# Performance work log

Hardware: AMD Instinct MI355X
Metric: run time of the kernel (lower is better)

The kernel has to match this reference:

```python
import jax, jax.numpy as jnp
import numpy as np

DIM = 768
HEADS = 12
HEAD_DIM = DIM // HEADS  # 64
B, T = 4, 2048


def setup_inputs() -> dict:
    key = jax.random.key(0)
    k1, k2, k3 = jax.random.split(key, 3)
    x = jax.random.normal(k1, (B, T, DIM), dtype=jnp.float32)
    w_qkv = jax.random.normal(k2, (DIM, 3 * DIM), dtype=jnp.float32) * (DIM ** -0.5)
    w_out = jax.random.normal(k3, (DIM, DIM), dtype=jnp.float32) * (DIM ** -0.5)
    b_out = jnp.zeros((DIM,), dtype=jnp.float32)
    return {"x": x, "w_qkv": w_qkv, "w_out": w_out, "b_out": b_out}


def reference(x, w_qkv, w_out, b_out):
    b, t, _ = x.shape
    # fused QKV projection (no bias)
    xp = x @ w_qkv                               # (b, t, 3*dim)
    # faithful to einops 'b t (d k h) -> k b h t d' with k=3, h=HEADS
    xp = xp.reshape(b, t, HEAD_DIM, 3, HEADS)
    qkv = jnp.transpose(xp, (3, 0, 4, 1, 2))     # (3, b, h, t, d)
    q, k, v = qkv[0], qkv[1], qkv[2]
    scores = jnp.einsum('bhid,bhjd->bhij', q, k) * (HEAD_DIM ** -0.5)
    attn = jax.nn.softmax(scores, axis=-1)
    out = jnp.einsum('bhij,bhjd->bhid', attn, v)  # (b, h, t, d)
    out = jnp.transpose(out, (0, 2, 1, 3)).reshape(b, t, HEADS * HEAD_DIM)
    return out @ w_out + b_out
```

## Files before the change

### kernel.cpp

```cpp
#include <hip/hip_runtime.h>
#include <hip/hip_bf16.h>


typedef short short8 __attribute__((ext_vector_type(8)));
typedef _Float16 half8 __attribute__((ext_vector_type(8)));
typedef _Float16 half2v __attribute__((ext_vector_type(2)));
typedef float f32x16 __attribute__((ext_vector_type(16)));
typedef unsigned int uint4v __attribute__((ext_vector_type(4)));
typedef unsigned short ushort8v __attribute__((ext_vector_type(8)));
typedef unsigned short ushort4v __attribute__((ext_vector_type(4)));
typedef unsigned short ushort;

__device__ __forceinline__ ushort f2h(float x) {
    _Float16 h = (_Float16)x;
    return __builtin_bit_cast(ushort, h);
}
__device__ __forceinline__ unsigned pk2h(float lo, float hi) {
    return __builtin_bit_cast(unsigned, __builtin_amdgcn_cvt_pkrtz(lo, hi));
}
__device__ __forceinline__ float dot2acc(unsigned pair, float acc) {
    const half2v ones = {(_Float16)1.0f, (_Float16)1.0f};
    return __builtin_amdgcn_fdot2(__builtin_bit_cast(half2v, pair), ones, acc, false);
}
__device__ __forceinline__ short8 ldfrag(const ushort* buf, int row, int slotLogical) {
    int phys = slotLogical ^ (row & 7);
    return *reinterpret_cast<const short8*>(&buf[row * 64 + phys * 8]);
}
__device__ __forceinline__ f32x16 mfma16(half8 a, half8 b, f32x16 c) {
    return __builtin_amdgcn_mfma_f32_32x32x16_f16(a, b, c, 0, 0, 0);
}
__device__ __forceinline__ half8 ldfragh(const ushort* buf, int row, int slotLogical) {
    return __builtin_bit_cast(half8, ldfrag(buf, row, slotLogical));
}
__device__ __forceinline__ void gload16(const ushort* g, ushort* l) {
    __builtin_amdgcn_global_load_lds((__attribute__((address_space(1))) void*)g,
                                     (__attribute__((address_space(3))) void*)l, 16, 0, 0);
}

__global__ __launch_bounds__(256) void prep_all(const float* __restrict__ x,
                                                const float* __restrict__ wqkv,
                                                const float* __restrict__ wout,
                                                ushort* __restrict__ Xh,
                                                ushort* __restrict__ Wt,
                                                ushort* __restrict__ Wo) {
    int b = blockIdx.x;
    if (b < 3072) {
        long i8 = (long)(b * 256 + threadIdx.x) * 8;
        float4 v0 = *reinterpret_cast<const float4*>(&x[i8]);
        float4 v1 = *reinterpret_cast<const float4*>(&x[i8 + 4]);
        float v[8] = {v0.x, v0.y, v0.z, v0.w, v1.x, v1.y, v1.z, v1.w};
        ushort8v hh;
#pragma unroll
        for (int j = 0; j < 8; ++j) hh[j] = f2h(v[j]);
        *reinterpret_cast<ushort8v*>(&Xh[i8]) = hh;
    } else if (b < 3072 + 864) {
        int id = (b - 3072) * 256 + threadIdx.x;
        int n = id % 2304;
        int oct = id / 2304;
        int g = n >> 6, d = n & 63;
        int col = d * 36 + g;
        ushort8v hh;
#pragma unroll
        for (int i = 0; i < 8; ++i) hh[i] = f2h(wqkv[(long)(8 * oct + i) * 2304 + col]);
        *reinterpret_cast<ushort8v*>(&Wt[(long)n * 768 + 8 * oct]) = hh;
    } else {
        int id = (b - 3936) * 256 + threadIdx.x;
        int n = id % 768;
        int oct = id / 768;
        ushort8v hh;
#pragma unroll
        for (int i = 0; i < 8; ++i) hh[i] = f2h(wout[(long)(8 * oct + i) * 768 + n]);
        *reinterpret_cast<ushort8v*>(&Wo[(long)n * 768 + 8 * oct]) = hh;
    }
}

__device__ __forceinline__ void gemm_core(const ushort* __restrict__ A,
                                          const ushort* __restrict__ Bt,
                                          long aBase, long bBase,
                                          ushort* sA, ushort* sB, f32x16 (&acc)[2][2]) {
    const int tid = threadIdx.x;
    const int lane = tid & 63, w = tid >> 6;
    const int c31 = lane & 31, g1 = lane >> 5;
    const int wr = w >> 1, wc = w & 1;
    const int srow_in_chunk = lane >> 3;
    for (int k0 = 0; k0 < 768; k0 += 64) {
        __syncthreads();
#pragma unroll
        for (int t = 0; t < 4; ++t) {
            int row = w * 32 + t * 8 + srow_in_chunk;
            int sl = (lane & 7) ^ (row & 7);
            long goff = (long)row * 768 + k0 + sl * 8;
            int ldst = (w * 32 + t * 8) * 64;
            gload16(&A[aBase + goff], &sA[ldst]);
            gload16(&Bt[bBase + goff], &sB[ldst]);
        }
        __syncthreads();
#pragma unroll
        for (int ks = 0; ks < 4; ++ks) {
            half8 ah[2], bh[2];
#pragma unroll
            for (int i = 0; i < 2; ++i) {
                ah[i] = ldfragh(sA, wr * 64 + i * 32 + c31, 2 * ks + g1);
                bh[i] = ldfragh(sB, wc * 64 + i * 32 + c31, 2 * ks + g1);
            }
#pragma unroll
            for (int mi = 0; mi < 2; ++mi)
#pragma unroll
                for (int nj = 0; nj < 2; ++nj)
                    acc[mi][nj] = mfma16(ah[mi], bh[nj], acc[mi][nj]);
        }
    }
}

__global__ __launch_bounds__(256) void gemm_qkv(const ushort* __restrict__ Xh,
                                                const ushort* __restrict__ Wt,
                                                ushort* __restrict__ Qf,
                                                ushort* __restrict__ Kf,
                                                ushort* __restrict__ Vt) {
    __shared__ ushort sA[128 * 64];
    __shared__ ushort sB[128 * 64];
    const int by0 = blockIdx.y * 128, bx0 = blockIdx.x * 128;
    f32x16 acc[2][2] = {};
    gemm_core(Xh, Wt, (long)by0 * 768, (long)bx0 * 768, sA, sB, acc);

    const int tid = threadIdx.x, lane = tid & 63, w = tid >> 6;
    const int c31 = lane & 31, g1 = lane >> 5;
    const int wr = w >> 1, wc = w & 1;
    const int bb = by0 >> 11, tb = by0 & 2047;
#pragma unroll
    for (int nj = 0; nj < 2; ++nj) {
        int n = bx0 + wc * 64 + nj * 32 + c31;
        int gg = n >> 6;
        int d = n & 63;
        if (gg < 24) {
            int kq = gg >= 12;
            int hh = gg - kq * 12;
            ushort* Dst = kq ? Kf : Qf;
            float sc = kq ? 0.1803368801111204f : 1.0f;
            long cb = ((long)(bb * 12 + hh) * 2048) * 64 + d;
#pragma unroll
            for (int mi = 0; mi < 2; ++mi)
#pragma unroll
                for (int r = 0; r < 16; ++r) {
                    int t = tb + wr * 64 + mi * 32 + (r & 3) + 8 * (r >> 2) + 4 * g1;
                    Dst[cb + (long)t * 64] = f2h(acc[mi][nj][r] * sc);
                }
        } else {
            int hh = gg - 24;
            long vb = ((long)(bb * 12 + hh) * 64 + d) * 2048;
#pragma unroll
            for (int mi = 0; mi < 2; ++mi)
#pragma unroll
                for (int rq = 0; rq < 4; ++rq) {
                    int tq = tb + wr * 64 + mi * 32 + 8 * rq + 4 * g1;
                    ushort4v vv;
#pragma unroll
                    for (int j = 0; j < 4; ++j) vv[j] = f2h(acc[mi][nj][4 * rq + j]);
                    *reinterpret_cast<ushort4v*>(&Vt[vb + tq]) = vv;
                }
        }
    }
}

__global__ __launch_bounds__(256) void flash_attn(const ushort* __restrict__ Qf,
                                                  const ushort* __restrict__ Kf,
                                                  const ushort* __restrict__ Vt,
                                                  ushort* __restrict__ Of) {
    __shared__ ushort Ks[3][64 * 64];
    __shared__ ushort Vs[3][64 * 64];
    const int tid = threadIdx.x;
    const int w = tid >> 6;
    const int lane = tid & 63;
    const int c = lane & 31, g1 = lane >> 5;
    const int wgid = blockIdx.x;
    const int xblk = (wgid >> 3) & 15;
    const int bh = (wgid & 7) + 8 * (wgid >> 7);
    const int t0 = xblk * 128 + w * 32;
    const long hb = (long)bh * 2048 * 64;

    half8 qh[4];
    {
        const long qrow = hb + (long)(t0 + c) * 64;
#pragma unroll
        for (int ks = 0; ks < 4; ++ks)
            qh[ks] = __builtin_bit_cast(half8, *reinterpret_cast<const short8*>(&Qf[qrow + ks * 16 + g1 * 8]));
    }

    const int r0 = tid >> 3, sl = tid & 7, r1 = r0 + 32;
    const int off0 = r0 * 64 + ((sl ^ (r0 & 7)) * 8);
    const int off1 = r1 * 64 + ((sl ^ (r1 & 7)) * 8);

    {
        short8 k00 = *reinterpret_cast<const short8*>(&Kf[hb + (long)r0 * 64 + sl * 8]);
        short8 k01 = *reinterpret_cast<const short8*>(&Kf[hb + (long)r1 * 64 + sl * 8]);
        short8 v00 = *reinterpret_cast<const short8*>(&Vt[hb + (long)r0 * 2048 + sl * 8]);
        short8 v01 = *reinterpret_cast<const short8*>(&Vt[hb + (long)r1 * 2048 + sl * 8]);
        short8 k10 = *reinterpret_cast<const short8*>(&Kf[hb + (long)(64 + r0) * 64 + sl * 8]);
        short8 k11 = *reinterpret_cast<const short8*>(&Kf[hb + (long)(64 + r1) * 64 + sl * 8]);
        short8 v10 = *reinterpret_cast<const short8*>(&Vt[hb + (long)r0 * 2048 + 64 + sl * 8]);
        short8 v11 = *reinterpret_cast<const short8*>(&Vt[hb + (long)r1 * 2048 + 64 + sl * 8]);
        *reinterpret_cast<short8*>(&Ks[0][off0]) = k00;
        *reinterpret_cast<short8*>(&Ks[0][off1]) = k01;
        *reinterpret_cast<short8*>(&Vs[0][off0]) = v00;
        *reinterpret_cast<short8*>(&Vs[0][off1]) = v01;
        *reinterpret_cast<short8*>(&Ks[1][off0]) = k10;
        *reinterpret_cast<short8*>(&Ks[1][off1]) = k11;
        *reinterpret_cast<short8*>(&Vs[1][off0]) = v10;
        *reinterpret_cast<short8*>(&Vs[1][off1]) = v11;
    }
    __syncthreads();

    const ushort* kst0 = &Kf[hb + (long)(128 + r0) * 64 + sl * 8];
    const ushort* kst1 = &Kf[hb + (long)(128 + r1) * 64 + sl * 8];
    const ushort* vst0 = &Vt[hb + (long)r0 * 2048 + 128 + sl * 8];
    const ushort* vst1 = &Vt[hb + (long)r1 * 2048 + 128 + sl * 8];

    f32x16 s0 = {}, s1 = {};
#pragma unroll
    for (int ks = 0; ks < 4; ++ks) {
        int slot = 2 * ks + g1;
        half8 k0f = ldfragh(&Ks[0][0], c, slot);
        half8 k1f = ldfragh(&Ks[0][0], 32 + c, slot);
        s0 = mfma16(k0f, qh[ks], s0);
        s1 = mfma16(k1f, qh[ks], s1);
    }

    f32x16 o0 = {}, o1 = {};
    float lrun = 0.f;
    int p = 0;

    for (int j = 0; j < 32; ++j) {
        const bool hasN1 = j + 1 < 32;
        const bool hasN2 = j + 2 < 32;
        const int p1 = (p + 1 == 3) ? 0 : p + 1;
        const int p2 = (p + 2 >= 3) ? p + 2 - 3 : p + 2;

        f32x16 n0 = {}, n1 = {};
        if (hasN1) {
            __builtin_amdgcn_s_setprio(1);
#pragma unroll
            for (int ks = 0; ks < 4; ++ks) {
                int slot = 2 * ks + g1;
                half8 k0f = ldfragh(&Ks[p1][0], c, slot);
                half8 k1f = ldfragh(&Ks[p1][0], 32 + c, slot);
                n0 = mfma16(k0f, qh[ks], n0);
                n1 = mfma16(k1f, qh[ks], n1);
            }
            __builtin_amdgcn_s_setprio(0);
        }

        short8 pk0, pk1, pv0, pv1;
        if (hasN2) {
            pk0 = *reinterpret_cast<const short8*>(kst0);
            pk1 = *reinterpret_cast<const short8*>(kst1);
            pv0 = *reinterpret_cast<const short8*>(vst0);
            pv1 = *reinterpret_cast<const short8*>(vst1);
            kst0 += 4096; kst1 += 4096;
            vst0 += 64;   vst1 += 64;
        }

#pragma unroll
        for (int r = 0; r < 16; ++r) {
            s0[r] = exp2f(s0[r]);
            s1[r] = exp2f(s1[r]);
        }

        __builtin_amdgcn_s_setprio(1);
#pragma unroll
        for (int ks = 0; ks < 4; ++ks) {
            const int b8 = (ks & 1) * 8;
            uint4v dv;
#pragma unroll
            for (int mi = 0; mi < 2; ++mi) {
                float aLo = (ks < 2) ? s0[2 * mi + b8] : s1[2 * mi + b8];
                float aHi = (ks < 2) ? s0[2 * mi + b8 + 1] : s1[2 * mi + b8 + 1];
                float bLo = (ks < 2) ? s0[2 * mi + b8 + 4] : s1[2 * mi + b8 + 4];
                float bHi = (ks < 2) ? s0[2 * mi + b8 + 5] : s1[2 * mi + b8 + 5];
                unsigned xA = pk2h(aLo, aHi);
                unsigned xB = pk2h(bLo, bHi);
                lrun = dot2acc(xA, lrun);
                lrun = dot2acc(xB, lrun);
                auto rr = __builtin_amdgcn_permlane32_swap(xA, xB, false, false);
                dv[mi] = rr[0];
                dv[2 + mi] = rr[1];
            }
            half8 pb = __builtin_bit_cast(half8, dv);
            int slot = 2 * ks + g1;
            half8 va0 = ldfragh(&Vs[p][0], c, slot);
            half8 va1 = ldfragh(&Vs[p][0], 32 + c, slot);
            o0 = mfma16(va0, pb, o0);
            o1 = mfma16(va1, pb, o1);
        }
        __builtin_amdgcn_s_setprio(0);

        if (hasN2) {
            *reinterpret_cast<short8*>(&Ks[p2][off0]) = pk0;
            *reinterpret_cast<short8*>(&Ks[p2][off1]) = pk1;
            *reinterpret_cast<short8*>(&Vs[p2][off0]) = pv0;
            *reinterpret_cast<short8*>(&Vs[p2][off1]) = pv1;
        }
        __syncthreads();

        s0 = n0; s1 = n1;
        p = p1;
    }

    const float ltot = lrun + __shfl_xor(lrun, 32);
    const float inv = 1.0f / ltot;
    const int bb = bh / 12, h = bh - bb * 12;
    const long obase = ((long)(bb * 2048 + t0 + c)) * 768 + h * 64;
#pragma unroll
    for (int m = 0; m < 4; ++m) {
        int d0 = 8 * m + 4 * g1;
        ushort4v a, b;
#pragma unroll
        for (int j = 0; j < 4; ++j) {
            a[j] = f2h(o0[4 * m + j] * inv);
            b[j] = f2h(o1[4 * m + j] * inv);
        }
        *reinterpret_cast<ushort4v*>(&Of[obase + d0]) = a;
        *reinterpret_cast<ushort4v*>(&Of[obase + 32 + d0]) = b;
    }
}

__global__ __launch_bounds__(256) void gemm_out(const ushort* __restrict__ Of,
                                                const ushort* __restrict__ Wo,
                                                const float* __restrict__ bias,
                                                float* __restrict__ Cout) {
    __shared__ ushort sA[128 * 64];
    __shared__ ushort sB[128 * 64];
    const int by0 = blockIdx.y * 128, bx0 = blockIdx.x * 128;
    f32x16 acc[2][2] = {};
    gemm_core(Of, Wo, (long)by0 * 768, (long)bx0 * 768, sA, sB, acc);

    const int tid = threadIdx.x, lane = tid & 63, w = tid >> 6;
    const int c31 = lane & 31, g1 = lane >> 5;
    const int wr = w >> 1, wc = w & 1;
#pragma unroll
    for (int nj = 0; nj < 2; ++nj) {
        int n = bx0 + wc * 64 + nj * 32 + c31;
        float bv = bias[n];
#pragma unroll
        for (int mi = 0; mi < 2; ++mi)
#pragma unroll
            for (int r = 0; r < 16; ++r) {
                int row = by0 + wr * 64 + mi * 32 + (r & 3) + 8 * (r >> 2) + 4 * g1;
                Cout[(long)row * 768 + n] = acc[mi][nj][r] + bv;
            }
    }
}

extern "C" void kernel_launch(void* const* d_in, const int* in_sizes, int n_in,
                              void* d_out, int out_size, void* d_ws, size_t ws_size,
                              hipStream_t stream) {
    const float* x     = (const float*)d_in[0];
    const float* w_qkv = (const float*)d_in[1];
    const float* w_out = (const float*)d_in[2];
    const float* b_out = (const float*)d_in[3];
    float* out = (float*)d_out;

    const long U = 12582912;
    char* p = (char*)d_ws;
    ushort* Xh = (ushort*)(p);
    ushort* Wt = (ushort*)(p + U);
    ushort* Wo = (ushort*)(p + U + 3538944);
    ushort* Qf = (ushort*)(p + U + 4718592);
    ushort* Kf = Qf + 6291456;
    ushort* Vt = Kf + 6291456;
    ushort* Of = Xh;

    prep_all  <<<4224, 256, 0, stream>>>(x, w_qkv, w_out, Xh, Wt, Wo);
    gemm_qkv  <<<dim3(18, 64), 256, 0, stream>>>(Xh, Wt, Qf, Kf, Vt);
    flash_attn<<<768, 256, 0, stream>>>(Qf, Kf, Vt, Of);
    gemm_out  <<<dim3(6, 64), 256, 0, stream>>>(Of, Wo, b_out, out);
}
```

Before: 183.2 us.

## Split attention over two key halves and combine partial outputs

Result: slower. 209.2 us (+14.1%).

```diff
diff --git a/kernel.cpp b/kernel.cpp
--- a/kernel.cpp
+++ b/kernel.cpp
@@ -15,6 +15,9 @@
     _Float16 h = (_Float16)x;
     return __builtin_bit_cast(ushort, h);
 }
+__device__ __forceinline__ float h2f(ushort u) {
+    return (float)__builtin_bit_cast(_Float16, u);
+}
 __device__ __forceinline__ unsigned pk2h(float lo, float hi) {
     return __builtin_bit_cast(unsigned, __builtin_amdgcn_cvt_pkrtz(lo, hi));
 }
@@ -31,6 +34,9 @@
 }
 __device__ __forceinline__ half8 ldfragh(const ushort* buf, int row, int slotLogical) {
     return __builtin_bit_cast(half8, ldfrag(buf, row, slotLogical));
+}
+__device__ __forceinline__ half8 ldh(const ushort* p) {
+    return __builtin_bit_cast(half8, *reinterpret_cast<const short8*>(p));
 }
 __device__ __forceinline__ void gload16(const ushort* g, ushort* l) {
     __builtin_amdgcn_global_load_lds((__attribute__((address_space(1))) void*)g,
@@ -165,25 +171,30 @@
 __global__ __launch_bounds__(256) void flash_attn(const ushort* __restrict__ Qf,
                                                   const ushort* __restrict__ Kf,
                                                   const ushort* __restrict__ Vt,
-                                                  ushort* __restrict__ Of) {
-    __shared__ ushort Ks[3][64 * 64];
-    __shared__ ushort Vs[3][64 * 64];
+                                                  ushort* __restrict__ Op0,
+                                                  ushort* __restrict__ Op1,
+                                                  float* __restrict__ lp0,
+                                                  float* __restrict__ lp1) {
+    __shared__ ushort Ks[2][64 * 64];
     const int tid = threadIdx.x;
     const int w = tid >> 6;
     const int lane = tid & 63;
     const int c = lane & 31, g1 = lane >> 5;
     const int wgid = blockIdx.x;
-    const int xblk = (wgid >> 3) & 15;
-    const int bh = (wgid & 7) + 8 * (wgid >> 7);
+    const int inner = (wgid >> 3) & 31;
+    const int xblk = inner >> 1;
+    const int kh = inner & 1;
+    const int bh = (wgid & 7) + 8 * (wgid >> 8);
     const int t0 = xblk * 128 + w * 32;
     const long hb = (long)bh * 2048 * 64;
+    const int jbase = kh * 1024;
 
     half8 qh[4];
     {
         const long qrow = hb + (long)(t0 + c) * 64;
 #pragma unroll
         for (int ks = 0; ks < 4; ++ks)
-            qh[ks] = __builtin_bit_cast(half8, *reinterpret_cast<const short8*>(&Qf[qrow + ks * 16 + g1 * 8]));
+            qh[ks] = ldh(&Qf[qrow + ks * 16 + g1 * 8]);
     }
 
     const int r0 = tid >> 3, sl = tid & 7, r1 = r0 + 32;
@@ -191,72 +202,48 @@
     const int off1 = r1 * 64 + ((sl ^ (r1 & 7)) * 8);
 
     {
-        short8 k00 = *reinterpret_cast<const short8*>(&Kf[hb + (long)r0 * 64 + sl * 8]);
-        short8 k01 = *reinterpret_cast<const short8*>(&Kf[hb + (long)r1 * 64 + sl * 8]);
-        short8 v00 = *reinterpret_cast<const short8*>(&Vt[hb + (long)r0 * 2048 + sl * 8]);
-        short8 v01 = *reinterpret_cast<const short8*>(&Vt[hb + (long)r1 * 2048 + sl * 8]);
-        short8 k10 = *reinterpret_cast<const short8*>(&Kf[hb + (long)(64 + r0) * 64 + sl * 8]);
-        short8 k11 = *reinterpret_cast<const short8*>(&Kf[hb + (long)(64 + r1) * 64 + sl * 8]);
-        short8 v10 = *reinterpret_cast<const short8*>(&Vt[hb + (long)r0 * 2048 + 64 + sl * 8]);
-        short8 v11 = *reinterpret_cast<const short8*>(&Vt[hb + (long)r1 * 2048 + 64 + sl * 8]);
-        *reinterpret_cast<short8*>(&Ks[0][off0]) = k00;
-        *reinterpret_cast<short8*>(&Ks[0][off1]) = k01;
-        *reinterpret_cast<short8*>(&Vs[0][off0]) = v00;
-        *reinterpret_cast<short8*>(&Vs[0][off1]) = v01;
-        *reinterpret_cast<short8*>(&Ks[1][off0]) = k10;
-        *reinterpret_cast<short8*>(&Ks[1][off1]) = k11;
-        *reinterpret_cast<short8*>(&Vs[1][off0]) = v10;
-        *reinterpret_cast<short8*>(&Vs[1][off1]) = v11;
-    }
+        short8 a = *reinterpret_cast<const short8*>(&Kf[hb + (long)(jbase + r0) * 64 + sl * 8]);
+        short8 b = *reinterpret_cast<const short8*>(&Kf[hb + (long)(jbase + r1) * 64 + sl * 8]);
+        *reinterpret_cast<short8*>(&Ks[0][off0]) = a;
+        *reinterpret_cast<short8*>(&Ks[0][off1]) = b;
+    }
+    const ushort* kst0 = &Kf[hb + (long)(jbase + 64 + r0) * 64 + sl * 8];
+    const ushort* kst1 = &Kf[hb + (long)(jbase + 64 + r1) * 64 + sl * 8];
+    const ushort* vp0 = &Vt[hb + (long)c * 2048 + jbase + g1 * 8];
+    const ushort* vp1 = vp0 + 32 * 2048;
     __syncthreads();
-
-    const ushort* kst0 = &Kf[hb + (long)(128 + r0) * 64 + sl * 8];
-    const ushort* kst1 = &Kf[hb + (long)(128 + r1) * 64 + sl * 8];
-    const ushort* vst0 = &Vt[hb + (long)r0 * 2048 + 128 + sl * 8];
-    const ushort* vst1 = &Vt[hb + (long)r1 * 2048 + 128 + sl * 8];
-
-    f32x16 s0 = {}, s1 = {};
-#pragma unroll
-    for (int ks = 0; ks < 4; ++ks) {
-        int slot = 2 * ks + g1;
-        half8 k0f = ldfragh(&Ks[0][0], c, slot);
-        half8 k1f = ldfragh(&Ks[0][0], 32 + c, slot);
-        s0 = mfma16(k0f, qh[ks], s0);
-        s1 = mfma16(k1f, qh[ks], s1);
-    }
 
     f32x16 o0 = {}, o1 = {};
     float lrun = 0.f;
-    int p = 0;
-
-    for (int j = 0; j < 32; ++j) {
-        const bool hasN1 = j + 1 < 32;
-        const bool hasN2 = j + 2 < 32;
-        const int p1 = (p + 1 == 3) ? 0 : p + 1;
-        const int p2 = (p + 2 >= 3) ? p + 2 - 3 : p + 2;
-
-        f32x16 n0 = {}, n1 = {};
-        if (hasN1) {
-            __builtin_amdgcn_s_setprio(1);
-#pragma unroll
-            for (int ks = 0; ks < 4; ++ks) {
-                int slot = 2 * ks + g1;
-                half8 k0f = ldfragh(&Ks[p1][0], c, slot);
-                half8 k1f = ldfragh(&Ks[p1][0], 32 + c, slot);
-                n0 = mfma16(k0f, qh[ks], n0);
-                n1 = mfma16(k1f, qh[ks], n1);
-            }
-            __builtin_amdgcn_s_setprio(0);
-        }
-
-        short8 pk0, pk1, pv0, pv1;
-        if (hasN2) {
+    int cur = 0;
+
+    for (int j = 0; j < 16; ++j) {
+        half8 vf0[4], vf1[4];
+        vf0[0] = ldh(vp0);      vf1[0] = ldh(vp1);
+        vf0[1] = ldh(vp0 + 16); vf1[1] = ldh(vp1 + 16);
+
+        f32x16 s0 = {}, s1 = {};
+        __builtin_amdgcn_s_setprio(1);
+#pragma unroll
+        for (int ks = 0; ks < 4; ++ks) {
+            int slot = 2 * ks + g1;
+            half8 k0f = ldfragh(&Ks[cur][0], c, slot);
+            half8 k1f = ldfragh(&Ks[cur][0], 32 + c, slot);
+            s0 = mfma16(k0f, qh[ks], s0);
+            s1 = mfma16(k1f, qh[ks], s1);
+        }
+        __builtin_amdgcn_s_setprio(0);
+
+        vf0[2] = ldh(vp0 + 32); vf1[2] = ldh(vp1 + 32);
+        vf0[3] = ldh(vp0 + 48); vf1[3] = ldh(vp1 + 48);
+        vp0 += 64; vp1 += 64;
+
+        short8 pk0, pk1;
+        const bool nxt = j + 1 < 16;
+        if (nxt) {
             pk0 = *reinterpret_cast<const short8*>(kst0);
             pk1 = *reinterpret_cast<const short8*>(kst1);
-            pv0 = *reinterpret_cast<const short8*>(vst0);
-            pv1 = *reinterpret_cast<const short8*>(vst1);
             kst0 += 4096; kst1 += 4096;
-            vst0 += 64;   vst1 += 64;
         }
 
 #pragma unroll
@@ -285,41 +272,67 @@
                 dv[2 + mi] = rr[1];
             }
             half8 pb = __builtin_bit_cast(half8, dv);
-            int slot = 2 * ks + g1;
-            half8 va0 = ldfragh(&Vs[p][0], c, slot);
-            half8 va1 = ldfragh(&Vs[p][0], 32 + c, slot);
-            o0 = mfma16(va0, pb, o0);
-            o1 = mfma16(va1, pb, o1);
+            o0 = mfma16(vf0[ks], pb, o0);
+            o1 = mfma16(vf1[ks], pb, o1);
         }
         __builtin_amdgcn_s_setprio(0);
 
-        if (hasN2) {
-            *reinterpret_cast<short8*>(&Ks[p2][off0]) = pk0;
-            *reinterpret_cast<short8*>(&Ks[p2][off1]) = pk1;
-            *reinterpret_cast<short8*>(&Vs[p2][off0]) = pv0;
-            *reinterpret_cast<short8*>(&Vs[p2][off1]) = pv1;
+        if (nxt) {
+            *reinterpret_cast<short8*>(&Ks[cur ^ 1][off0]) = pk0;
+            *reinterpret_cast<short8*>(&Ks[cur ^ 1][off1]) = pk1;
         }
         __syncthreads();
-
-        s0 = n0; s1 = n1;
-        p = p1;
+        cur ^= 1;
     }
 
     const float ltot = lrun + __shfl_xor(lrun, 32);
-    const float inv = 1.0f / ltot;
+    ushort* Op = kh ? Op1 : Op0;
+    float* lp = kh ? lp1 : lp0;
+    const long pbase = ((long)bh * 64) * 2048 + t0 + c;
+#pragma unroll
+    for (int r = 0; r < 16; ++r) {
+        int d0 = (r & 3) + 8 * (r >> 2) + 4 * g1;
+        Op[pbase + (long)d0 * 2048] = f2h(o0[r]);
+        Op[pbase + (long)(32 + d0) * 2048] = f2h(o1[r]);
+    }
+    if (g1 == 0) lp[(long)bh * 2048 + t0 + c] = ltot;
+}
+
+__global__ __launch_bounds__(256) void combine(const ushort* __restrict__ Op0,
+                                               const ushort* __restrict__ Op1,
+                                               const float* __restrict__ lp0,
+                                               const float* __restrict__ lp1,
+                                               ushort* __restrict__ Of) {
+    __shared__ float linv[64];
+    __shared__ ushort tile[64][72];
+    const int bh = blockIdx.x >> 5;
+    const int tb = blockIdx.x & 31;
+    const int t0 = tb * 64;
+    const int tid = threadIdx.x;
+    if (tid < 64)
+        linv[tid] = 1.0f / (lp0[(long)bh * 2048 + t0 + tid] + lp1[(long)bh * 2048 + t0 + tid]);
+    __syncthreads();
+#pragma unroll
+    for (int it = 0; it < 2; ++it) {
+        int u = tid + 256 * it;
+        int d = u & 63, tg = u >> 6;
+        long base = ((long)bh * 64 + d) * 2048 + t0 + tg * 8;
+        ushort8v a = *reinterpret_cast<const ushort8v*>(&Op0[base]);
+        ushort8v b = *reinterpret_cast<const ushort8v*>(&Op1[base]);
+#pragma unroll
+        for (int j = 0; j < 8; ++j)
+            tile[tg * 8 + j][d] = f2h((h2f(a[j]) + h2f(b[j])) * linv[tg * 8 + j]);
+    }
+    __syncthreads();
     const int bb = bh / 12, h = bh - bb * 12;
-    const long obase = ((long)(bb * 2048 + t0 + c)) * 768 + h * 64;
-#pragma unroll
-    for (int m = 0; m < 4; ++m) {
-        int d0 = 8 * m + 4 * g1;
-        ushort4v a, b;
-#pragma unroll
-        for (int j = 0; j < 4; ++j) {
-            a[j] = f2h(o0[4 * m + j] * inv);
-            b[j] = f2h(o1[4 * m + j] * inv);
-        }
-        *reinterpret_cast<ushort4v*>(&Of[obase + d0]) = a;
-        *reinterpret_cast<ushort4v*>(&Of[obase + 32 + d0]) = b;
+#pragma unroll
+    for (int it = 0; it < 2; ++it) {
+        int u = tid + 256 * it;
+        int dg = u & 7, t = u >> 3;
+        ushort8v v;
+#pragma unroll
+        for (int j = 0; j < 8; ++j) v[j] = tile[t][dg * 8 + j];
+        *reinterpret_cast<ushort8v*>(&Of[((long)(bb * 2048) + t0 + t) * 768 + h * 64 + dg * 8]) = v;
     }
 }
 
@@ -361,16 +374,21 @@
 
     const long U = 12582912;
     char* p = (char*)d_ws;
-    ushort* Xh = (ushort*)(p);
-    ushort* Wt = (ushort*)(p + U);
-    ushort* Wo = (ushort*)(p + U + 3538944);
-    ushort* Qf = (ushort*)(p + U + 4718592);
-    ushort* Kf = Qf + 6291456;
-    ushort* Vt = Kf + 6291456;
-    ushort* Of = Xh;
+    ushort* Xh  = (ushort*)(p);
+    ushort* Wt  = (ushort*)(p + U);
+    ushort* Wo  = (ushort*)(p + U + 3538944);
+    ushort* Qf  = (ushort*)(p + U + 4718592);
+    ushort* Kf  = Qf + 6291456;
+    ushort* Vt  = Kf + 6291456;
+    ushort* Op0 = Vt + 6291456;
+    ushort* Op1 = Op0 + 6291456;
+    float*  lp0 = (float*)(Op1 + 6291456);
+    float*  lp1 = lp0 + 98304;
+    ushort* Of  = Xh;
 
     prep_all  <<<4224, 256, 0, stream>>>(x, w_qkv, w_out, Xh, Wt, Wo);
     gemm_qkv  <<<dim3(18, 64), 256, 0, stream>>>(Xh, Wt, Qf, Kf, Vt);
-    flash_attn<<<768, 256, 0, stream>>>(Qf, Kf, Vt, Of);
+    flash_attn<<<1536, 256, 0, stream>>>(Qf, Kf, Vt, Op0, Op1, lp0, lp1);
+    combine   <<<1536, 256, 0, stream>>>(Op0, Op1, lp0, lp1, Of);
     gemm_out  <<<dim3(6, 64), 256, 0, stream>>>(Of, Wo, b_out, out);
 }
```

## Enlarge GEMM tiles to 256x128 with 512 threads; ping-pong flash-attn score registers

Applied to the files above, without the earlier changes.

Measured after the change: 205.5 us. 12.1% more time.

```diff
diff --git a/kernel.cpp b/kernel.cpp
--- a/kernel.cpp
+++ b/kernel.cpp
@@ -82,17 +82,20 @@
     const int lane = tid & 63, w = tid >> 6;
     const int c31 = lane & 31, g1 = lane >> 5;
     const int wr = w >> 1, wc = w & 1;
-    const int srow_in_chunk = lane >> 3;
+    const int rch = lane >> 3;
     for (int k0 = 0; k0 < 768; k0 += 64) {
         __syncthreads();
 #pragma unroll
         for (int t = 0; t < 4; ++t) {
-            int row = w * 32 + t * 8 + srow_in_chunk;
+            int row = w * 32 + t * 8 + rch;
             int sl = (lane & 7) ^ (row & 7);
-            long goff = (long)row * 768 + k0 + sl * 8;
-            int ldst = (w * 32 + t * 8) * 64;
-            gload16(&A[aBase + goff], &sA[ldst]);
-            gload16(&Bt[bBase + goff], &sB[ldst]);
+            gload16(&A[aBase + (long)row * 768 + k0 + sl * 8], &sA[(w * 32 + t * 8) * 64]);
+        }
+#pragma unroll
+        for (int t = 0; t < 2; ++t) {
+            int row = w * 16 + t * 8 + rch;
+            int sl = (lane & 7) ^ (row & 7);
+            gload16(&Bt[bBase + (long)row * 768 + k0 + sl * 8], &sB[(w * 16 + t * 8) * 64]);
         }
         __syncthreads();
 #pragma unroll
@@ -112,14 +115,14 @@
     }
 }
 
-__global__ __launch_bounds__(256) void gemm_qkv(const ushort* __restrict__ Xh,
+__global__ __launch_bounds__(512) void gemm_qkv(const ushort* __restrict__ Xh,
                                                 const ushort* __restrict__ Wt,
                                                 ushort* __restrict__ Qf,
                                                 ushort* __restrict__ Kf,
                                                 ushort* __restrict__ Vt) {
-    __shared__ ushort sA[128 * 64];
+    __shared__ ushort sA[256 * 64];
     __shared__ ushort sB[128 * 64];
-    const int by0 = blockIdx.y * 128, bx0 = blockIdx.x * 128;
+    const int by0 = blockIdx.y * 256, bx0 = blockIdx.x * 128;
     f32x16 acc[2][2] = {};
     gemm_core(Xh, Wt, (long)by0 * 768, (long)bx0 * 768, sA, sB, acc);
 
@@ -215,36 +218,46 @@
     const ushort* vst0 = &Vt[hb + (long)r0 * 2048 + 128 + sl * 8];
     const ushort* vst1 = &Vt[hb + (long)r1 * 2048 + 128 + sl * 8];
 
-    f32x16 s0 = {}, s1 = {};
-#pragma unroll
-    for (int ks = 0; ks < 4; ++ks) {
-        int slot = 2 * ks + g1;
-        half8 k0f = ldfragh(&Ks[0][0], c, slot);
-        half8 k1f = ldfragh(&Ks[0][0], 32 + c, slot);
-        s0 = mfma16(k0f, qh[ks], s0);
-        s1 = mfma16(k1f, qh[ks], s1);
+    const f32x16 kzero = {};
+
+    f32x16 s0, s1;
+    {
+        half8 k0f = ldfragh(&Ks[0][0], c, g1);
+        half8 k1f = ldfragh(&Ks[0][0], 32 + c, g1);
+        s0 = mfma16(k0f, qh[0], kzero);
+        s1 = mfma16(k1f, qh[0], kzero);
+#pragma unroll
+        for (int ks = 1; ks < 4; ++ks) {
+            int slot = 2 * ks + g1;
+            k0f = ldfragh(&Ks[0][0], c, slot);
+            k1f = ldfragh(&Ks[0][0], 32 + c, slot);
+            s0 = mfma16(k0f, qh[ks], s0);
+            s1 = mfma16(k1f, qh[ks], s1);
+        }
     }
 
     f32x16 o0 = {}, o1 = {};
     float lrun = 0.f;
     int p = 0;
 
-    for (int j = 0; j < 32; ++j) {
-        const bool hasN1 = j + 1 < 32;
-        const bool hasN2 = j + 2 < 32;
+    auto fiter = [&](bool hasN1, bool hasN2, f32x16& cs0, f32x16& cs1,
+                     f32x16& ns0, f32x16& ns1) {
         const int p1 = (p + 1 == 3) ? 0 : p + 1;
         const int p2 = (p + 2 >= 3) ? p + 2 - 3 : p + 2;
 
-        f32x16 n0 = {}, n1 = {};
         if (hasN1) {
             __builtin_amdgcn_s_setprio(1);
-#pragma unroll
-            for (int ks = 0; ks < 4; ++ks) {
+            half8 k0f = ldfragh(&Ks[p1][0], c, g1);
+            half8 k1f = ldfragh(&Ks[p1][0], 32 + c, g1);
+            ns0 = mfma16(k0f, qh[0], kzero);
+            ns1 = mfma16(k1f, qh[0], kzero);
+#pragma unroll
+            for (int ks = 1; ks < 4; ++ks) {
                 int slot = 2 * ks + g1;
-                half8 k0f = ldfragh(&Ks[p1][0], c, slot);
-                half8 k1f = ldfragh(&Ks[p1][0], 32 + c, slot);
-                n0 = mfma16(k0f, qh[ks], n0);
-                n1 = mfma16(k1f, qh[ks], n1);
+                k0f = ldfragh(&Ks[p1][0], c, slot);
+                k1f = ldfragh(&Ks[p1][0], 32 + c, slot);
+                ns0 = mfma16(k0f, qh[ks], ns0);
+                ns1 = mfma16(k1f, qh[ks], ns1);
             }
             __builtin_amdgcn_s_setprio(0);
         }
@@ -261,8 +274,8 @@
 
 #pragma unroll
         for (int r = 0; r < 16; ++r) {
-            s0[r] = exp2f(s0[r]);
-            s1[r] = exp2f(s1[r]);
+            cs0[r] = exp2f(cs0[r]);
+            cs1[r] = exp2f(cs1[r]);
         }
 
         __builtin_amdgcn_s_setprio(1);
@@ -272,10 +285,10 @@
             uint4v dv;
 #pragma unroll
             for (int mi = 0; mi < 2; ++mi) {
-                float aLo = (ks < 2) ? s0[2 * mi + b8] : s1[2 * mi + b8];
-                float aHi = (ks < 2) ? s0[2 * mi + b8 + 1] : s1[2 * mi + b8 + 1];
-                float bLo = (ks < 2) ? s0[2 * mi + b8 + 4] : s1[2 * mi + b8 + 4];
-                float bHi = (ks < 2) ? s0[2 * mi + b8 + 5] : s1[2 * mi + b8 + 5];
+                float aLo = (ks < 2) ? cs0[2 * mi + b8] : cs1[2 * mi + b8];
+                float aHi = (ks < 2) ? cs0[2 * mi + b8 + 1] : cs1[2 * mi + b8 + 1];
+                float bLo = (ks < 2) ? cs0[2 * mi + b8 + 4] : cs1[2 * mi + b8 + 4];
+                float bHi = (ks < 2) ? cs0[2 * mi + b8 + 5] : cs1[2 * mi + b8 + 5];
                 unsigned xA = pk2h(aLo, aHi);
                 unsigned xB = pk2h(bLo, bHi);
                 lrun = dot2acc(xA, lrun);
@@ -300,9 +313,13 @@
             *reinterpret_cast<short8*>(&Vs[p2][off1]) = pv1;
         }
         __syncthreads();
-
-        s0 = n0; s1 = n1;
         p = p1;
+    };
+
+    f32x16 n0, n1;
+    for (int j = 0; j < 32; j += 2) {
+        fiter(true, j + 2 < 32, s0, s1, n0, n1);
+        fiter(j + 2 < 32, j + 3 < 32, n0, n1, s0, s1);
     }
 
     const float ltot = lrun + __shfl_xor(lrun, 32);
@@ -323,13 +340,13 @@
     }
 }
 
-__global__ __launch_bounds__(256) void gemm_out(const ushort* __restrict__ Of,
+__global__ __launch_bounds__(512) void gemm_out(const ushort* __restrict__ Of,
                                                 const ushort* __restrict__ Wo,
                                                 const float* __restrict__ bias,
                                                 float* __restrict__ Cout) {
-    __shared__ ushort sA[128 * 64];
+    __shared__ ushort sA[256 * 64];
     __shared__ ushort sB[128 * 64];
-    const int by0 = blockIdx.y * 128, bx0 = blockIdx.x * 128;
+    const int by0 = blockIdx.y * 256, bx0 = blockIdx.x * 128;
     f32x16 acc[2][2] = {};
     gemm_core(Of, Wo, (long)by0 * 768, (long)bx0 * 768, sA, sB, acc);
 
@@ -370,7 +387,7 @@
     ushort* Of = Xh;
 
     prep_all  <<<4224, 256, 0, stream>>>(x, w_qkv, w_out, Xh, Wt, Wo);
-    gemm_qkv  <<<dim3(18, 64), 256, 0, stream>>>(Xh, Wt, Qf, Kf, Vt);
+    gemm_qkv  <<<dim3(18, 32), 512, 0, stream>>>(Xh, Wt, Qf, Kf, Vt);
     flash_attn<<<768, 256, 0, stream>>>(Qf, Kf, Vt, Of);
-    gemm_out  <<<dim3(6, 64), 256, 0, stream>>>(Of, Wo, b_out, out);
-}
+    gemm_out  <<<dim3(6, 32), 512, 0, stream>>>(Of, Wo, b_out, out);
+}
```

## Stream K/V tiles directly from global to LDS with async direct loads

Applied to the files above, without the earlier changes.

After: 183.0 us. No clear change (-0.1%).

```diff
diff --git a/kernel.cpp b/kernel.cpp
--- a/kernel.cpp
+++ b/kernel.cpp
@@ -186,34 +186,27 @@
             qh[ks] = __builtin_bit_cast(half8, *reinterpret_cast<const short8*>(&Qf[qrow + ks * 16 + g1 * 8]));
     }
 
-    const int r0 = tid >> 3, sl = tid & 7, r1 = r0 + 32;
-    const int off0 = r0 * 64 + ((sl ^ (r0 & 7)) * 8);
-    const int off1 = r1 * 64 + ((sl ^ (r1 & 7)) * 8);
-
-    {
-        short8 k00 = *reinterpret_cast<const short8*>(&Kf[hb + (long)r0 * 64 + sl * 8]);
-        short8 k01 = *reinterpret_cast<const short8*>(&Kf[hb + (long)r1 * 64 + sl * 8]);
-        short8 v00 = *reinterpret_cast<const short8*>(&Vt[hb + (long)r0 * 2048 + sl * 8]);
-        short8 v01 = *reinterpret_cast<const short8*>(&Vt[hb + (long)r1 * 2048 + sl * 8]);
-        short8 k10 = *reinterpret_cast<const short8*>(&Kf[hb + (long)(64 + r0) * 64 + sl * 8]);
-        short8 k11 = *reinterpret_cast<const short8*>(&Kf[hb + (long)(64 + r1) * 64 + sl * 8]);
-        short8 v10 = *reinterpret_cast<const short8*>(&Vt[hb + (long)r0 * 2048 + 64 + sl * 8]);
-        short8 v11 = *reinterpret_cast<const short8*>(&Vt[hb + (long)r1 * 2048 + 64 + sl * 8]);
-        *reinterpret_cast<short8*>(&Ks[0][off0]) = k00;
-        *reinterpret_cast<short8*>(&Ks[0][off1]) = k01;
-        *reinterpret_cast<short8*>(&Vs[0][off0]) = v00;
-        *reinterpret_cast<short8*>(&Vs[0][off1]) = v01;
-        *reinterpret_cast<short8*>(&Ks[1][off0]) = k10;
-        *reinterpret_cast<short8*>(&Ks[1][off1]) = k11;
-        *reinterpret_cast<short8*>(&Vs[1][off0]) = v10;
-        *reinterpret_cast<short8*>(&Vs[1][off1]) = v11;
+    const int srow = lane >> 3;
+    const int scol = (lane & 7) ^ srow;
+    const int kr0 = w * 16 + srow;
+    const int kr1 = kr0 + 8;
+    const int ld0 = (w * 16) * 64;
+    const int ld1 = (w * 16 + 8) * 64;
+    const ushort* kg0 = &Kf[hb + (long)kr0 * 64 + scol * 8];
+    const ushort* kg1 = &Kf[hb + (long)kr1 * 64 + scol * 8];
+    const ushort* vg0 = &Vt[hb + (long)kr0 * 2048 + scol * 8];
+    const ushort* vg1 = &Vt[hb + (long)kr1 * 2048 + scol * 8];
+
+#pragma unroll
+    for (int t = 0; t < 2; ++t) {
+        gload16(kg0, &Ks[t][ld0]);
+        gload16(kg1, &Ks[t][ld1]);
+        gload16(vg0, &Vs[t][ld0]);
+        gload16(vg1, &Vs[t][ld1]);
+        kg0 += 4096; kg1 += 4096;
+        vg0 += 64;   vg1 += 64;
     }
     __syncthreads();
-
-    const ushort* kst0 = &Kf[hb + (long)(128 + r0) * 64 + sl * 8];
-    const ushort* kst1 = &Kf[hb + (long)(128 + r1) * 64 + sl * 8];
-    const ushort* vst0 = &Vt[hb + (long)r0 * 2048 + 128 + sl * 8];
-    const ushort* vst1 = &Vt[hb + (long)r1 * 2048 + 128 + sl * 8];
 
     f32x16 s0 = {}, s1 = {};
 #pragma unroll
@@ -234,6 +227,15 @@
         const bool hasN2 = j + 2 < 32;
         const int p1 = (p + 1 == 3) ? 0 : p + 1;
         const int p2 = (p + 2 >= 3) ? p + 2 - 3 : p + 2;
+
+        if (hasN2) {
+            gload16(kg0, &Ks[p2][ld0]);
+            gload16(kg1, &Ks[p2][ld1]);
+            gload16(vg0, &Vs[p2][ld0]);
+            gload16(vg1, &Vs[p2][ld1]);
+            kg0 += 4096; kg1 += 4096;
+            vg0 += 64;   vg1 += 64;
+        }
 
         f32x16 n0 = {}, n1 = {};
         if (hasN1) {
@@ -247,16 +249,6 @@
                 n1 = mfma16(k1f, qh[ks], n1);
             }
             __builtin_amdgcn_s_setprio(0);
-        }
-
-        short8 pk0, pk1, pv0, pv1;
-        if (hasN2) {
-            pk0 = *reinterpret_cast<const short8*>(kst0);
-            pk1 = *reinterpret_cast<const short8*>(kst1);
-            pv0 = *reinterpret_cast<const short8*>(vst0);
-            pv1 = *reinterpret_cast<const short8*>(vst1);
-            kst0 += 4096; kst1 += 4096;
-            vst0 += 64;   vst1 += 64;
         }
 
 #pragma unroll
@@ -293,12 +285,6 @@
         }
         __builtin_amdgcn_s_setprio(0);
 
-        if (hasN2) {
-            *reinterpret_cast<short8*>(&Ks[p2][off0]) = pk0;
-            *reinterpret_cast<short8*>(&Ks[p2][off1]) = pk1;
-            *reinterpret_cast<short8*>(&Vs[p2][off0]) = pv0;
-            *reinterpret_cast<short8*>(&Vs[p2][off1]) = pv1;
-        }
         __syncthreads();
 
         s0 = n0; s1 = n1;
```
